# Kernel optimization log

Hardware: AMD Instinct MI355X
Metric: run time of the kernel (lower is better)

The kernel has to match this reference:

```python
import math
import jax, jax.numpy as jnp
import numpy as np

SPARSE_RATIO = 0.6  # module default sparse_ratio


def setup_inputs() -> dict:
    key = jax.random.key(0)
    k1, k2, k3 = jax.random.split(key, 3)
    B, N, C = 64, 4096, 512
    tokens = jax.random.normal(k1, (B, N, C), dtype=jnp.float32)
    attention_x = jax.random.normal(k2, (B, N), dtype=jnp.float32)
    attention_y = jax.random.normal(k3, (B, N), dtype=jnp.float32)
    return {"tokens": tokens, "attention_x": attention_x, "attention_y": attention_y}


def reference(tokens, attention_x, attention_y):
    # tokens: (B, N, C); attention_x/attention_y: (B, N)
    B, N, C = tokens.shape
    num_keep = max(1, math.ceil(N * SPARSE_RATIO))  # static

    # simplified score fusion (use_paper_version=False path)
    score = attention_x + attention_y  # (B, N)

    # full descending sort -> top-k keep indices + sorted scores
    order = jnp.argsort(-score, axis=1)                      # (B, N)
    score_sort = jnp.take_along_axis(score, order, axis=1)   # (B, N) descending

    keep_policy = order[:, :num_keep]                        # (B, K)
    select_tokens = jnp.take_along_axis(
        tokens, keep_policy[:, :, None], axis=1)             # (B, K, C)

    # hard decision mask: 1 at kept positions
    batch_idx = jnp.arange(B)[:, None]
    score_mask = jnp.zeros_like(score).at[batch_idx, keep_policy].set(1.0)  # (B, N)

    # softmax-weighted merge of dropped tokens into one extra token
    non_keep_policy = order[:, num_keep:]                    # (B, N-K)
    non_tokens = jnp.take_along_axis(
        tokens, non_keep_policy[:, :, None], axis=1)         # (B, N-K, C)
    non_w = jax.nn.softmax(score_sort[:, num_keep:], axis=1)[:, :, None]
    extra_token = jnp.sum(non_tokens * non_w, axis=1, keepdims=True)  # (B, 1, C)

    return select_tokens, extra_token, score_mask
```

## Files before the change

### kernel.cpp

```cpp
#include <hip/hip_runtime.h>

#define B_DIM 64
#define N_TOK 4096
#define C_DIM 512
#define C4 128
#define NUM_KEEP 2458
#define NON_KEEP 1638
#define SPLITS 16

__device__ __forceinline__ float ts_decode_key(unsigned kd) {
    unsigned ka = ~kd;
    unsigned u = (ka & 0x80000000u) ? (ka ^ 0x80000000u) : ~ka;
    return __uint_as_float(u);
}

__global__ __launch_bounds__(512) void ts_sort_kernel(
    const float* __restrict__ ax, const float* __restrict__ ay,
    int* __restrict__ order, float* __restrict__ weights,
    float* __restrict__ mask)
{
    __shared__ unsigned long long keys[N_TOK];
    __shared__ float red[8];
    __shared__ float sh_vals[2];
    const int b = blockIdx.x;
    const int tid = threadIdx.x;
    const int nthr = blockDim.x;

    const float* axb = ax + b * N_TOK;
    const float* ayb = ay + b * N_TOK;
    for (int i = tid; i < N_TOK; i += nthr) {
        float s = axb[i] + ayb[i];
        unsigned u = __float_as_uint(s);
        unsigned kd = (u & 0x80000000u) ? u : ~(u | 0x80000000u);
        keys[i] = ((unsigned long long)kd << 32) | (unsigned)i;
    }
    __syncthreads();

    for (int k = 2; k <= N_TOK; k <<= 1) {
        for (int j = k >> 1; j > 0; j >>= 1) {
            for (int i = tid; i < N_TOK; i += nthr) {
                int ixj = i ^ j;
                if (ixj > i) {
                    unsigned long long a = keys[i];
                    unsigned long long c = keys[ixj];
                    bool sw = ((i & k) == 0) ? (a > c) : (a < c);
                    if (sw) { keys[i] = c; keys[ixj] = a; }
                }
            }
            __syncthreads();
        }
    }

    if (tid == 0) sh_vals[0] = ts_decode_key((unsigned)(keys[NUM_KEEP] >> 32));
    __syncthreads();
    const float m = sh_vals[0];

    float local = 0.f;
    for (int p = tid; p < N_TOK; p += nthr) {
        unsigned long long kk = keys[p];
        int idx = (int)(kk & 0xFFFFFFFFu);
        order[b * N_TOK + p] = idx;
        mask[b * N_TOK + idx] = (p < NUM_KEEP) ? 1.0f : 0.0f;
        if (p >= NUM_KEEP) local += expf(ts_decode_key((unsigned)(kk >> 32)) - m);
    }
    for (int off = 32; off > 0; off >>= 1) local += __shfl_down(local, off);
    if ((tid & 63) == 0) red[tid >> 6] = local;
    __syncthreads();
    if (tid == 0) {
        float s = 0.f;
        for (int w = 0; w < 512 / 64; ++w) s += red[w];
        sh_vals[1] = 1.0f / s;
    }
    __syncthreads();
    const float inv = sh_vals[1];
    for (int p = NUM_KEEP + tid; p < N_TOK; p += nthr) {
        float s = ts_decode_key((unsigned)(keys[p] >> 32));
        weights[b * NON_KEEP + (p - NUM_KEEP)] = expf(s - m) * inv;
    }
}

__global__ __launch_bounds__(256) void ts_gather_kernel(
    const float4* __restrict__ tokens, const int* __restrict__ order,
    float4* __restrict__ sel)
{
    int row = blockIdx.x * 2 + (threadIdx.x >> 7);
    int lane = threadIdx.x & 127;
    int b = row / NUM_KEEP;
    int k = row - b * NUM_KEEP;
    int idx = order[b * N_TOK + k];
    sel[(long long)row * C4 + lane] =
        tokens[((long long)(b * N_TOK) + idx) * C4 + lane];
}

__global__ __launch_bounds__(128) void ts_wsum_kernel(
    const float4* __restrict__ tokens, const int* __restrict__ order,
    const float* __restrict__ weights, float4* __restrict__ partials)
{
    int b = blockIdx.x / SPLITS;
    int split = blockIdx.x - b * SPLITS;
    int lane = threadIdx.x;
    const int per = (NON_KEEP + SPLITS - 1) / SPLITS;
    int j0 = split * per;
    int j1 = j0 + per; if (j1 > NON_KEEP) j1 = NON_KEEP;
    float4 acc = make_float4(0.f, 0.f, 0.f, 0.f);
    for (int j = j0; j < j1; ++j) {
        int idx = order[b * N_TOK + NUM_KEEP + j];
        float w = weights[b * NON_KEEP + j];
        float4 t = tokens[((long long)(b * N_TOK) + idx) * C4 + lane];
        acc.x += w * t.x; acc.y += w * t.y; acc.z += w * t.z; acc.w += w * t.w;
    }
    partials[(b * SPLITS + split) * C4 + lane] = acc;
}

__global__ __launch_bounds__(128) void ts_reduce_kernel(
    const float4* __restrict__ partials, float4* __restrict__ extra)
{
    int b = blockIdx.x;
    int lane = threadIdx.x;
    float4 acc = make_float4(0.f, 0.f, 0.f, 0.f);
    for (int s = 0; s < SPLITS; ++s) {
        float4 t = partials[(b * SPLITS + s) * C4 + lane];
        acc.x += t.x; acc.y += t.y; acc.z += t.z; acc.w += t.w;
    }
    extra[b * C4 + lane] = acc;
}

extern "C" void kernel_launch(void* const* d_in, const int* in_sizes, int n_in,
                              void* d_out, int out_size, void* d_ws, size_t ws_size,
                              hipStream_t stream) {
    const float* tokens = (const float*)d_in[0];
    const float* ax     = (const float*)d_in[1];
    const float* ay     = (const float*)d_in[2];

    float* out   = (float*)d_out;
    float* sel   = out;
    float* extra = out + (long long)B_DIM * NUM_KEEP * C_DIM;
    float* mask  = extra + B_DIM * C_DIM;

    char* ws = (char*)d_ws;
    int*   order    = (int*)ws;
    float* weights  = (float*)(ws + (size_t)B_DIM * N_TOK * 4);
    float* partials = (float*)(ws + (size_t)B_DIM * N_TOK * 4
                                  + (size_t)B_DIM * NON_KEEP * 4);

    ts_sort_kernel<<<B_DIM, 512, 0, stream>>>(ax, ay, order, weights, mask);
    ts_gather_kernel<<<(B_DIM * NUM_KEEP) / 2, 256, 0, stream>>>(
        (const float4*)tokens, order, (float4*)sel);
    ts_wsum_kernel<<<B_DIM * SPLITS, 128, 0, stream>>>(
        (const float4*)tokens, order, weights, (float4*)partials);
    ts_reduce_kernel<<<B_DIM, 128, 0, stream>>>(
        (const float4*)partials, (float4*)extra);
}
```

Before: 897.1 us.

## Replace bitonic sort with rank counting and fuse gather with weighted sum

After: 879.2 us. -2.0%, faster.

```diff
diff --git a/kernel.cpp b/kernel.cpp
--- a/kernel.cpp
+++ b/kernel.cpp
@@ -6,110 +6,142 @@
 #define C4 128
 #define NUM_KEEP 2458
 #define NON_KEEP 1638
-#define SPLITS 16
+#define SPLITS 32
+#define PER_SPLIT 52
+#define WSUM_BLOCKS (B_DIM * SPLITS / 4)
+#define GATHER_BLOCKS 2048
+#define GATHER_GROUPS (GATHER_BLOCKS * 4)
+#define TOTAL_SEL_ROWS (B_DIM * NUM_KEEP)
 
-__device__ __forceinline__ float ts_decode_key(unsigned kd) {
-    unsigned ka = ~kd;
-    unsigned u = (ka & 0x80000000u) ? (ka ^ 0x80000000u) : ~ka;
-    return __uint_as_float(u);
+typedef float f32x4_t __attribute__((ext_vector_type(4)));
+
+__device__ __forceinline__ float4 nt_load4(const float4* p) {
+    f32x4_t v = __builtin_nontemporal_load((const f32x4_t*)p);
+    return make_float4(v.x, v.y, v.z, v.w);
+}
+__device__ __forceinline__ void nt_store4(float4* p, float4 v) {
+    f32x4_t w = {v.x, v.y, v.z, v.w};
+    __builtin_nontemporal_store(w, (f32x4_t*)p);
 }
 
-__global__ __launch_bounds__(512) void ts_sort_kernel(
+__global__ __launch_bounds__(256) void ts_rank_kernel(
     const float* __restrict__ ax, const float* __restrict__ ay,
-    int* __restrict__ order, float* __restrict__ weights,
+    int* __restrict__ order, float* __restrict__ svals,
     float* __restrict__ mask)
 {
-    __shared__ unsigned long long keys[N_TOK];
-    __shared__ float red[8];
-    __shared__ float sh_vals[2];
-    const int b = blockIdx.x;
+    __shared__ __align__(16) unsigned long long keys[N_TOK];
+    const int blk = blockIdx.x;
+    const int b   = blk >> 2;
+    const int sp  = blk & 3;
     const int tid = threadIdx.x;
-    const int nthr = blockDim.x;
 
     const float* axb = ax + b * N_TOK;
     const float* ayb = ay + b * N_TOK;
-    for (int i = tid; i < N_TOK; i += nthr) {
+
+    unsigned long long myk[4];
+    float ms[4];
+    #pragma unroll
+    for (int k = 0; k < 16; ++k) {
+        int i = k * 256 + tid;
         float s = axb[i] + ayb[i];
         unsigned u = __float_as_uint(s);
         unsigned kd = (u & 0x80000000u) ? u : ~(u | 0x80000000u);
-        keys[i] = ((unsigned long long)kd << 32) | (unsigned)i;
+        unsigned long long key = ((unsigned long long)kd << 32) | (unsigned)i;
+        keys[i] = key;
+        if ((k >> 2) == sp) { myk[k & 3] = key; ms[k & 3] = s; }
     }
     __syncthreads();
 
-    for (int k = 2; k <= N_TOK; k <<= 1) {
-        for (int j = k >> 1; j > 0; j >>= 1) {
-            for (int i = tid; i < N_TOK; i += nthr) {
-                int ixj = i ^ j;
-                if (ixj > i) {
-                    unsigned long long a = keys[i];
-                    unsigned long long c = keys[ixj];
-                    bool sw = ((i & k) == 0) ? (a > c) : (a < c);
-                    if (sw) { keys[i] = c; keys[ixj] = a; }
-                }
-            }
-            __syncthreads();
-        }
+    int ra0 = 0, ra1 = 0, ra2 = 0, ra3 = 0;
+    int rb0 = 0, rb1 = 0, rb2 = 0, rb3 = 0;
+    const ulonglong2* kp = (const ulonglong2*)keys;
+    #pragma unroll 4
+    for (int j = 0; j < N_TOK / 2; ++j) {
+        ulonglong2 kk = kp[j];
+        ra0 += (kk.x < myk[0]); rb0 += (kk.y < myk[0]);
+        ra1 += (kk.x < myk[1]); rb1 += (kk.y < myk[1]);
+        ra2 += (kk.x < myk[2]); rb2 += (kk.y < myk[2]);
+        ra3 += (kk.x < myk[3]); rb3 += (kk.y < myk[3]);
     }
+    int rank[4] = {ra0 + rb0, ra1 + rb1, ra2 + rb2, ra3 + rb3};
 
-    if (tid == 0) sh_vals[0] = ts_decode_key((unsigned)(keys[NUM_KEEP] >> 32));
-    __syncthreads();
-    const float m = sh_vals[0];
+    #pragma unroll
+    for (int e = 0; e < 4; ++e) {
+        int i = sp * 1024 + e * 256 + tid;
+        int r = rank[e];
+        order[b * N_TOK + r] = i;
+        svals[b * N_TOK + r] = ms[e];
+        mask [b * N_TOK + i] = (r < NUM_KEEP) ? 1.0f : 0.0f;
+    }
+}
+
+__global__ __launch_bounds__(512) void ts_weights_kernel(
+    const float* __restrict__ svals, float* __restrict__ weights)
+{
+    __shared__ float red[8];
+    __shared__ float sinv;
+    const int b = blockIdx.x;
+    const int tid = threadIdx.x;
+    const float m = svals[b * N_TOK + NUM_KEEP];
 
     float local = 0.f;
-    for (int p = tid; p < N_TOK; p += nthr) {
-        unsigned long long kk = keys[p];
-        int idx = (int)(kk & 0xFFFFFFFFu);
-        order[b * N_TOK + p] = idx;
-        mask[b * N_TOK + idx] = (p < NUM_KEEP) ? 1.0f : 0.0f;
-        if (p >= NUM_KEEP) local += expf(ts_decode_key((unsigned)(kk >> 32)) - m);
+    for (int p = tid; p < NON_KEEP; p += 512) {
+        float e = expf(svals[b * N_TOK + NUM_KEEP + p] - m);
+        weights[b * NON_KEEP + p] = e;
+        local += e;
     }
     for (int off = 32; off > 0; off >>= 1) local += __shfl_down(local, off);
     if ((tid & 63) == 0) red[tid >> 6] = local;
     __syncthreads();
     if (tid == 0) {
         float s = 0.f;
-        for (int w = 0; w < 512 / 64; ++w) s += red[w];
-        sh_vals[1] = 1.0f / s;
+        #pragma unroll
+        for (int w = 0; w < 8; ++w) s += red[w];
+        sinv = 1.0f / s;
     }
     __syncthreads();
-    const float inv = sh_vals[1];
-    for (int p = NUM_KEEP + tid; p < N_TOK; p += nthr) {
-        float s = ts_decode_key((unsigned)(keys[p] >> 32));
-        weights[b * NON_KEEP + (p - NUM_KEEP)] = expf(s - m) * inv;
-    }
+    const float inv = sinv;
+    for (int p = tid; p < NON_KEEP; p += 512)
+        weights[b * NON_KEEP + p] *= inv;
 }
 
-__global__ __launch_bounds__(256) void ts_gather_kernel(
+__global__ __launch_bounds__(512) void ts_heavy_kernel(
     const float4* __restrict__ tokens, const int* __restrict__ order,
-    float4* __restrict__ sel)
+    const float* __restrict__ weights, float4* __restrict__ sel,
+    float4* __restrict__ partials)
 {
-    int row = blockIdx.x * 2 + (threadIdx.x >> 7);
-    int lane = threadIdx.x & 127;
-    int b = row / NUM_KEEP;
-    int k = row - b * NUM_KEEP;
-    int idx = order[b * N_TOK + k];
-    sel[(long long)row * C4 + lane] =
-        tokens[((long long)(b * N_TOK) + idx) * C4 + lane];
-}
+    const int tid  = threadIdx.x;
+    const int g    = tid >> 7;
+    const int lane = tid & 127;
 
-__global__ __launch_bounds__(128) void ts_wsum_kernel(
-    const float4* __restrict__ tokens, const int* __restrict__ order,
-    const float* __restrict__ weights, float4* __restrict__ partials)
-{
-    int b = blockIdx.x / SPLITS;
-    int split = blockIdx.x - b * SPLITS;
-    int lane = threadIdx.x;
-    const int per = (NON_KEEP + SPLITS - 1) / SPLITS;
-    int j0 = split * per;
-    int j1 = j0 + per; if (j1 > NON_KEEP) j1 = NON_KEEP;
-    float4 acc = make_float4(0.f, 0.f, 0.f, 0.f);
-    for (int j = j0; j < j1; ++j) {
-        int idx = order[b * N_TOK + NUM_KEEP + j];
-        float w = weights[b * NON_KEEP + j];
-        float4 t = tokens[((long long)(b * N_TOK) + idx) * C4 + lane];
-        acc.x += w * t.x; acc.y += w * t.y; acc.z += w * t.z; acc.w += w * t.w;
+    if (blockIdx.x < WSUM_BLOCKS) {
+        int split = blockIdx.x * 4 + g;
+        int b = split >> 5;
+        int s = split & (SPLITS - 1);
+        int j0 = s * PER_SPLIT;
+        int j1 = j0 + PER_SPLIT; if (j1 > NON_KEEP) j1 = NON_KEEP;
+        const int*   ob = order + b * N_TOK + NUM_KEEP;
+        const float* wb = weights + b * NON_KEEP;
+        float4 acc = make_float4(0.f, 0.f, 0.f, 0.f);
+        #pragma unroll 2
+        for (int j = j0; j < j1; ++j) {
+            int idx = ob[j];
+            float w = wb[j];
+            float4 t = nt_load4(tokens + ((long long)(b * N_TOK) + idx) * C4 + lane);
+            acc.x += w * t.x; acc.y += w * t.y;
+            acc.z += w * t.z; acc.w += w * t.w;
+        }
+        partials[(long long)split * C4 + lane] = acc;
+    } else {
+        int grp = (blockIdx.x - WSUM_BLOCKS) * 4 + g;
+        for (int row = grp; row < TOTAL_SEL_ROWS; row += GATHER_GROUPS) {
+            int b = row / NUM_KEEP;
+            int k = row - b * NUM_KEEP;
+            int idx = order[b * N_TOK + k];
+            float4 v = nt_load4(tokens + ((long long)(b * N_TOK) + idx) * C4 + lane);
+            nt_store4(sel + (long long)row * C4 + lane, v);
+        }
     }
-    partials[(b * SPLITS + split) * C4 + lane] = acc;
 }
 
 __global__ __launch_bounds__(128) void ts_reduce_kernel(
@@ -118,8 +150,9 @@
     int b = blockIdx.x;
     int lane = threadIdx.x;
     float4 acc = make_float4(0.f, 0.f, 0.f, 0.f);
+    #pragma unroll
     for (int s = 0; s < SPLITS; ++s) {
-        float4 t = partials[(b * SPLITS + s) * C4 + lane];
+        float4 t = partials[(long long)(b * SPLITS + s) * C4 + lane];
         acc.x += t.x; acc.y += t.y; acc.z += t.z; acc.w += t.w;
     }
     extra[b * C4 + lane] = acc;
@@ -139,15 +172,14 @@
 
     char* ws = (char*)d_ws;
     int*   order    = (int*)ws;
-    float* weights  = (float*)(ws + (size_t)B_DIM * N_TOK * 4);
-    float* partials = (float*)(ws + (size_t)B_DIM * N_TOK * 4
-                                  + (size_t)B_DIM * NON_KEEP * 4);
+    float* svals    = (float*)(ws + (1u << 20));
+    float* weights  = (float*)(ws + (2u << 20));
+    float* partials = (float*)(ws + ((2u << 20) + (1u << 19)));
 
-    ts_sort_kernel<<<B_DIM, 512, 0, stream>>>(ax, ay, order, weights, mask);
-    ts_gather_kernel<<<(B_DIM * NUM_KEEP) / 2, 256, 0, stream>>>(
-        (const float4*)tokens, order, (float4*)sel);
-    ts_wsum_kernel<<<B_DIM * SPLITS, 128, 0, stream>>>(
-        (const float4*)tokens, order, weights, (float4*)partials);
+    ts_rank_kernel<<<B_DIM * 4, 256, 0, stream>>>(ax, ay, order, svals, mask);
+    ts_weights_kernel<<<B_DIM, 512, 0, stream>>>(svals, weights);
+    ts_heavy_kernel<<<WSUM_BLOCKS + GATHER_BLOCKS, 512, 0, stream>>>(
+        (const float4*)tokens, order, weights, (float4*)sel, (float4*)partials);
     ts_reduce_kernel<<<B_DIM, 128, 0, stream>>>(
         (const float4*)partials, (float4*)extra);
 }
```
